# Kernel optimization log

Hardware: AMD Instinct MI355X
Metric: run time of the kernel (lower is better)

## Reference

```python
import jax, jax.numpy as jnp
import numpy as np

N_ATOMS = 262144
N_MOL = 8192       # number of molecules (segments)
MAX_Z = 100        # atomic number vocabulary
MODEL_DIMS = 1024
OUTPUT_DIMS = 1


def setup_inputs() -> dict:
    key = jax.random.key(0)
    k1, k2, k3, k4, k5, k6, k7 = jax.random.split(key, 7)
    atomic_numbers = jax.random.randint(k1, (N_ATOMS,), 0, MAX_Z, dtype=jnp.int64 if jax.config.jax_enable_x64 else jnp.int32)
    pos = jax.random.normal(k2, (N_ATOMS, 3), dtype=jnp.float32)
    batch = jnp.sort(jax.random.randint(k3, (N_ATOMS,), 0, N_MOL, dtype=atomic_numbers.dtype))
    # learned parameters of atom_rr (embedding + position projection) and the head Linear
    embed = jax.random.normal(k4, (MAX_Z, MODEL_DIMS), dtype=jnp.float32) * 0.02
    w_pos = jax.random.normal(k5, (3, MODEL_DIMS), dtype=jnp.float32) * 0.02
    w = jax.random.normal(k6, (MODEL_DIMS, OUTPUT_DIMS), dtype=jnp.float32) * 0.02
    b = jnp.zeros((OUTPUT_DIMS,), dtype=jnp.float32)
    return {"atomic_numbers": atomic_numbers, "pos": pos, "batch": batch,
            "embed": embed, "w_pos": w_pos, "w": w, "b": b}


def reference(atomic_numbers, pos, batch, embed, w_pos, w, b):
    # Vectorized replacement for the per-molecule Python loop:
    # per-atom features, then segment-sum over molecule ids (data.batch).
    feats = embed[atomic_numbers] + pos @ w_pos          # [N_atoms, D]
    reduced = jax.ops.segment_sum(feats, batch, num_segments=N_MOL)  # [N_mol, D]
    return reduced @ w + b                               # [N_mol, output_dims]
```

## Files before the change

kernel.cpp:

```cpp
#include <hip/hip_runtime.h>

#define N_ATOMS 262144
#define N_MOL 8192
#define MAX_Z 100
#define MODEL_DIMS 1024


__global__ void prep_kernel(const float* __restrict__ embed,
                            const float* __restrict__ w_pos,
                            const float* __restrict__ w,
                            const float* __restrict__ b,
                            float* __restrict__ ewpw,
                            float* __restrict__ out) {
    const int blk = blockIdx.x;
    const int tid = threadIdx.x;
    __shared__ float red[256];

    if (blk < MAX_Z + 3) {
        const float* row = (blk < MAX_Z) ? (embed + (size_t)blk * MODEL_DIMS)
                                         : (w_pos + (size_t)(blk - MAX_Z) * MODEL_DIMS);
        float s = 0.f;
        for (int j = tid; j < MODEL_DIMS; j += 256)
            s += row[j] * w[j];
        red[tid] = s;
        __syncthreads();
        for (int off = 128; off > 0; off >>= 1) {
            if (tid < off) red[tid] += red[tid + off];
            __syncthreads();
        }
        if (tid == 0) ewpw[blk] = red[0];
    } else {
        const float bv = b[0];
        for (int i = tid; i < N_MOL; i += 256)
            out[i] = bv;
    }
}

__global__ void atom_kernel(const int* __restrict__ z,
                            const float* __restrict__ pos,
                            const int* __restrict__ batch,
                            const float* __restrict__ ewpw,
                            float* __restrict__ out) {
    const int i = blockIdx.x * blockDim.x + threadIdx.x;
    const float pw0 = ewpw[MAX_Z + 0];
    const float pw1 = ewpw[MAX_Z + 1];
    const float pw2 = ewpw[MAX_Z + 2];

    const int   id = batch[i];
    const int   zi = z[i];
    const float p0 = pos[3 * (size_t)i + 0];
    const float p1 = pos[3 * (size_t)i + 1];
    const float p2 = pos[3 * (size_t)i + 2];

    float v = ewpw[zi] + p0 * pw0 + p1 * pw1 + p2 * pw2;

    const int lane = threadIdx.x & 63;
    #pragma unroll
    for (int off = 1; off < 64; off <<= 1) {
        float vu = __shfl_up(v, off);
        int   iu = __shfl_up(id, off);
        if (lane >= off && iu == id) v += vu;
    }
    const int idn = __shfl_down(id, 1);
    const bool seg_last = (lane == 63) || (idn != id);
    if (seg_last) atomicAdd(&out[id], v);
}

extern "C" void kernel_launch(void* const* d_in, const int* in_sizes, int n_in,
                              void* d_out, int out_size, void* d_ws, size_t ws_size,
                              hipStream_t stream) {
    const int*   atomic_numbers = (const int*)d_in[0];
    const float* pos            = (const float*)d_in[1];
    const int*   batch          = (const int*)d_in[2];
    const float* embed          = (const float*)d_in[3];
    const float* w_pos          = (const float*)d_in[4];
    const float* w              = (const float*)d_in[5];
    const float* b              = (const float*)d_in[6];
    float*       out            = (float*)d_out;
    float*       ewpw           = (float*)d_ws;

    prep_kernel<<<MAX_Z + 4, 256, 0, stream>>>(embed, w_pos, w, b, ewpw, out);

    atom_kernel<<<N_ATOMS / 256, 256, 0, stream>>>(atomic_numbers, pos, batch,
                                                   ewpw, out);
}
```

Before: 11.62 us.

## Fuse prep and atom kernels into one persistent kernel with grid barrier

Merges the weight-dot-product prep kernel and the per-atom segment-reduction kernel into one 256-block launch. A global atomic counter acts as a grid-wide barrier between the two phases. Each block then handles 1024 atoms, four wave-sized chunks per wave, and reads the projected table from LDS. The aim is to drop one kernel launch and the gap between launches. In exchange it adds a spin-wait barrier that requires all 256 blocks to be co-resident, plus counter-reset logic.

Measured after the change: 27.06 us. +132.8%, slower.

```diff
diff --git a/kernel.cpp b/kernel.cpp
--- a/kernel.cpp
+++ b/kernel.cpp
@@ -3,67 +3,100 @@
 #define N_ATOMS 262144
 #define N_MOL 8192
 #define MAX_Z 100
-#define MODEL_DIMS 1024
+#define D 1024
+#define NBLK 256
+#define NTHR 256
+#define NDOT (MAX_Z + 3)
 
+__device__ int g_ready = 0;
+__device__ int g_done  = 0;
 
-__global__ void prep_kernel(const float* __restrict__ embed,
-                            const float* __restrict__ w_pos,
-                            const float* __restrict__ w,
-                            const float* __restrict__ b,
-                            float* __restrict__ ewpw,
-                            float* __restrict__ out) {
-    const int blk = blockIdx.x;
-    const int tid = threadIdx.x;
-    __shared__ float red[256];
+__global__ __launch_bounds__(NTHR) void fused_energy_kernel(
+    const int* __restrict__ z, const float* __restrict__ pos,
+    const int* __restrict__ batch,
+    const float* __restrict__ embed, const float* __restrict__ w_pos,
+    const float* __restrict__ w, const float* __restrict__ b,
+    float* __restrict__ out, float* __restrict__ ewpw)
+{
+    const int blk = blockIdx.x, tid = threadIdx.x;
+    __shared__ float red[NTHR];
+    __shared__ float ew_lds[NDOT];
 
-    if (blk < MAX_Z + 3) {
-        const float* row = (blk < MAX_Z) ? (embed + (size_t)blk * MODEL_DIMS)
-                                         : (w_pos + (size_t)(blk - MAX_Z) * MODEL_DIMS);
+    if (blk < NDOT) {
+        const float* row = (blk < MAX_Z) ? embed + (size_t)blk * D
+                                         : w_pos + (size_t)(blk - MAX_Z) * D;
         float s = 0.f;
-        for (int j = tid; j < MODEL_DIMS; j += 256)
-            s += row[j] * w[j];
+        for (int j = tid; j < D; j += NTHR) s += row[j] * w[j];
         red[tid] = s;
         __syncthreads();
-        for (int off = 128; off > 0; off >>= 1) {
+        for (int off = NTHR / 2; off > 0; off >>= 1) {
             if (tid < off) red[tid] += red[tid + off];
             __syncthreads();
         }
-        if (tid == 0) ewpw[blk] = red[0];
-    } else {
+        if (tid == 0)
+            __hip_atomic_store(&ewpw[blk], red[0], __ATOMIC_RELAXED,
+                               __HIP_MEMORY_SCOPE_AGENT);
+    }
+    {
         const float bv = b[0];
-        for (int i = tid; i < N_MOL; i += 256)
-            out[i] = bv;
+        const int base = blk * (N_MOL / NBLK);
+        if (tid < N_MOL / NBLK) out[base + tid] = bv;
     }
-}
 
-__global__ void atom_kernel(const int* __restrict__ z,
-                            const float* __restrict__ pos,
-                            const int* __restrict__ batch,
-                            const float* __restrict__ ewpw,
-                            float* __restrict__ out) {
-    const int i = blockIdx.x * blockDim.x + threadIdx.x;
-    const float pw0 = ewpw[MAX_Z + 0];
-    const float pw1 = ewpw[MAX_Z + 1];
-    const float pw2 = ewpw[MAX_Z + 2];
+    __syncthreads();
+    if (tid == 0) {
+        __threadfence();
+        __hip_atomic_fetch_add(&g_ready, 1, __ATOMIC_RELEASE,
+                               __HIP_MEMORY_SCOPE_AGENT);
+        while (__hip_atomic_load(&g_ready, __ATOMIC_RELAXED,
+                                 __HIP_MEMORY_SCOPE_AGENT) < NBLK)
+            __builtin_amdgcn_s_sleep(2);
+    }
+    __syncthreads();
 
-    const int   id = batch[i];
-    const int   zi = z[i];
-    const float p0 = pos[3 * (size_t)i + 0];
-    const float p1 = pos[3 * (size_t)i + 1];
-    const float p2 = pos[3 * (size_t)i + 2];
+    if (tid < NDOT)
+        ew_lds[tid] = __hip_atomic_load(&ewpw[tid], __ATOMIC_RELAXED,
+                                        __HIP_MEMORY_SCOPE_AGENT);
+    __syncthreads();
 
-    float v = ewpw[zi] + p0 * pw0 + p1 * pw1 + p2 * pw2;
+    const float pw0 = ew_lds[MAX_Z + 0];
+    const float pw1 = ew_lds[MAX_Z + 1];
+    const float pw2 = ew_lds[MAX_Z + 2];
+    const int lane = tid & 63;
+    const int wv   = tid >> 6;
+    const int wbase = blk * (N_ATOMS / NBLK) + wv * 256;
 
-    const int lane = threadIdx.x & 63;
     #pragma unroll
-    for (int off = 1; off < 64; off <<= 1) {
-        float vu = __shfl_up(v, off);
-        int   iu = __shfl_up(id, off);
-        if (lane >= off && iu == id) v += vu;
+    for (int t = 0; t < 4; ++t) {
+        const int i  = wbase + t * 64 + lane;
+        const int id = batch[i];
+        const int zi = z[i];
+        const float p0 = pos[3 * (size_t)i + 0];
+        const float p1 = pos[3 * (size_t)i + 1];
+        const float p2 = pos[3 * (size_t)i + 2];
+        float v = ew_lds[zi] + p0 * pw0 + p1 * pw1 + p2 * pw2;
+
+        #pragma unroll
+        for (int off = 1; off < 64; off <<= 1) {
+            float vu = __shfl_up(v, off);
+            int   iu = __shfl_up(id, off);
+            if (lane >= off && iu == id) v += vu;
+        }
+        const int idn = __shfl_down(id, 1);
+        if (lane == 63 || idn != id) atomicAdd(&out[id], v);
     }
-    const int idn = __shfl_down(id, 1);
-    const bool seg_last = (lane == 63) || (idn != id);
-    if (seg_last) atomicAdd(&out[id], v);
+
+    __syncthreads();
+    if (tid == 0) {
+        int old = __hip_atomic_fetch_add(&g_done, 1, __ATOMIC_ACQ_REL,
+                                         __HIP_MEMORY_SCOPE_AGENT);
+        if (old == NBLK - 1) {
+            __hip_atomic_store(&g_ready, 0, __ATOMIC_RELAXED,
+                               __HIP_MEMORY_SCOPE_AGENT);
+            __hip_atomic_store(&g_done, 0, __ATOMIC_RELAXED,
+                               __HIP_MEMORY_SCOPE_AGENT);
+        }
+    }
 }
 
 extern "C" void kernel_launch(void* const* d_in, const int* in_sizes, int n_in,
@@ -79,8 +112,6 @@
     float*       out            = (float*)d_out;
     float*       ewpw           = (float*)d_ws;
 
-    prep_kernel<<<MAX_Z + 4, 256, 0, stream>>>(embed, w_pos, w, b, ewpw, out);
-
-    atom_kernel<<<N_ATOMS / 256, 256, 0, stream>>>(atomic_numbers, pos, batch,
-                                                   ewpw, out);
+    fused_energy_kernel<<<NBLK, NTHR, 0, stream>>>(
+        atomic_numbers, pos, batch, embed, w_pos, w, b, out, ewpw);
 }
```

## Fuse table prep and segment sum into one kernel with per-block molecule ranges

Applied to the files above, without the earlier changes.

Merges the two launches into a single kernel. Each of 128 blocks recomputes the 103-entry dot-product table (embed·w, w_pos·w) redundantly in shared memory, then binary-searches the sorted batch array with wave ballots to find the atom range for its 64 molecules. It accumulates into shared memory and writes out once with the bias, removing global atomics and the out initialisation pass. The cost is redundant table computation per block (about 400KB of reads each, mostly from L2), and only 128 blocks to stream 262K atoms, which may underfill the GPU.

Result: slower. 14.59 us (+25.5%).

```diff
diff --git a/kernel.cpp b/kernel.cpp
--- a/kernel.cpp
+++ b/kernel.cpp
@@ -1,69 +1,104 @@
 #include <hip/hip_runtime.h>
 
 #define N_ATOMS 262144
-#define N_MOL 8192
-#define MAX_Z 100
-#define MODEL_DIMS 1024
+#define N_MOL   8192
+#define MAX_Z   100
+#define D       1024
+#define NDOT    (MAX_Z + 3)
+#define NBLK    128
+#define NTHR    512
+#define MPB     (N_MOL / NBLK)
+#define WAVES   (NTHR / 64)
 
+__global__ __launch_bounds__(NTHR) void fused_energy_kernel(
+    const int* __restrict__ z, const float* __restrict__ pos,
+    const int* __restrict__ batch,
+    const float* __restrict__ embed, const float* __restrict__ w_pos,
+    const float* __restrict__ w, const float* __restrict__ b,
+    float* __restrict__ out)
+{
+    const int blk  = blockIdx.x, tid = threadIdx.x;
+    const int lane = tid & 63,   wv  = tid >> 6;
+    __shared__ float tab[NDOT];
+    __shared__ float mol[MPB];
+    __shared__ int   bounds[2];
 
-__global__ void prep_kernel(const float* __restrict__ embed,
-                            const float* __restrict__ w_pos,
-                            const float* __restrict__ w,
-                            const float* __restrict__ b,
-                            float* __restrict__ ewpw,
-                            float* __restrict__ out) {
-    const int blk = blockIdx.x;
-    const int tid = threadIdx.x;
-    __shared__ float red[256];
+    if (tid < MPB) mol[tid] = 0.f;
 
-    if (blk < MAX_Z + 3) {
-        const float* row = (blk < MAX_Z) ? (embed + (size_t)blk * MODEL_DIMS)
-                                         : (w_pos + (size_t)(blk - MAX_Z) * MODEL_DIMS);
+    const int mol_base = blk * MPB;
+
+    if (wv < 2) {
+        const int V = mol_base + wv * MPB;
+        int lower;
+        int v1 = batch[lane * 4096];
+        int c1 = __popcll(__ballot(v1 < V));
+        if (c1 == 0) {
+            lower = 0;
+        } else {
+            int base1 = (c1 - 1) * 4096;
+            int idx2  = base1 + (lane + 1) * 64;
+            int v2    = (idx2 < N_ATOMS) ? batch[idx2] : 0x7fffffff;
+            int c2    = __popcll(__ballot(v2 < V));
+            int base2 = base1 + c2 * 64;
+            int idx3  = base2 + 1 + lane;
+            int v3    = (idx3 < N_ATOMS) ? batch[idx3] : 0x7fffffff;
+            int c3    = __popcll(__ballot(v3 < V));
+            lower = base2 + 1 + c3;
+        }
+        if (lane == 0) bounds[wv] = lower;
+    }
+
+    float4 wc[4];
+    #pragma unroll
+    for (int k = 0; k < 4; ++k)
+        wc[k] = *(const float4*)&w[4 * lane + 256 * k];
+
+    for (int r = wv; r < NDOT; r += WAVES) {
+        const float* row = (r < MAX_Z) ? embed + (size_t)r * D
+                                       : w_pos + (size_t)(r - MAX_Z) * D;
         float s = 0.f;
-        for (int j = tid; j < MODEL_DIMS; j += 256)
-            s += row[j] * w[j];
-        red[tid] = s;
-        __syncthreads();
-        for (int off = 128; off > 0; off >>= 1) {
-            if (tid < off) red[tid] += red[tid + off];
-            __syncthreads();
+        #pragma unroll
+        for (int k = 0; k < 4; ++k) {
+            float4 rv = *(const float4*)&row[4 * lane + 256 * k];
+            s += rv.x * wc[k].x + rv.y * wc[k].y + rv.z * wc[k].z + rv.w * wc[k].w;
         }
-        if (tid == 0) ewpw[blk] = red[0];
-    } else {
-        const float bv = b[0];
-        for (int i = tid; i < N_MOL; i += 256)
-            out[i] = bv;
+        #pragma unroll
+        for (int off = 32; off > 0; off >>= 1)
+            s += __shfl_xor(s, off);
+        if (lane == 0) tab[r] = s;
     }
-}
+    __syncthreads();
 
-__global__ void atom_kernel(const int* __restrict__ z,
-                            const float* __restrict__ pos,
-                            const int* __restrict__ batch,
-                            const float* __restrict__ ewpw,
-                            float* __restrict__ out) {
-    const int i = blockIdx.x * blockDim.x + threadIdx.x;
-    const float pw0 = ewpw[MAX_Z + 0];
-    const float pw1 = ewpw[MAX_Z + 1];
-    const float pw2 = ewpw[MAX_Z + 2];
+    const int lower = bounds[0], upper = bounds[1];
+    const float pw0 = tab[MAX_Z + 0];
+    const float pw1 = tab[MAX_Z + 1];
+    const float pw2 = tab[MAX_Z + 2];
 
-    const int   id = batch[i];
-    const int   zi = z[i];
-    const float p0 = pos[3 * (size_t)i + 0];
-    const float p1 = pos[3 * (size_t)i + 1];
-    const float p2 = pos[3 * (size_t)i + 2];
+    for (int base = lower; base < upper; base += NTHR) {
+        const int  i     = base + tid;
+        const bool valid = i < upper;
+        const int  ii    = valid ? i : (upper - 1);
 
-    float v = ewpw[zi] + p0 * pw0 + p1 * pw1 + p2 * pw2;
+        const int   id = valid ? batch[ii] : 0x7fffffff;
+        const int   zi = z[ii];
+        const float p0 = pos[3 * (size_t)ii + 0];
+        const float p1 = pos[3 * (size_t)ii + 1];
+        const float p2 = pos[3 * (size_t)ii + 2];
+        float v = valid ? (tab[zi] + p0 * pw0 + p1 * pw1 + p2 * pw2) : 0.f;
 
-    const int lane = threadIdx.x & 63;
-    #pragma unroll
-    for (int off = 1; off < 64; off <<= 1) {
-        float vu = __shfl_up(v, off);
-        int   iu = __shfl_up(id, off);
-        if (lane >= off && iu == id) v += vu;
+        #pragma unroll
+        for (int off = 1; off < 64; off <<= 1) {
+            float vu = __shfl_up(v, off);
+            int   iu = __shfl_up(id, off);
+            if (lane >= off && iu == id) v += vu;
+        }
+        const int idn = __shfl_down(id, 1);
+        if (valid && (lane == 63 || idn != id))
+            atomicAdd(&mol[id - mol_base], v);
     }
-    const int idn = __shfl_down(id, 1);
-    const bool seg_last = (lane == 63) || (idn != id);
-    if (seg_last) atomicAdd(&out[id], v);
+    __syncthreads();
+
+    if (tid < MPB) out[mol_base + tid] = b[0] + mol[tid];
 }
 
 extern "C" void kernel_launch(void* const* d_in, const int* in_sizes, int n_in,
@@ -77,10 +112,7 @@
     const float* w              = (const float*)d_in[5];
     const float* b              = (const float*)d_in[6];
     float*       out            = (float*)d_out;
-    float*       ewpw           = (float*)d_ws;
 
-    prep_kernel<<<MAX_Z + 4, 256, 0, stream>>>(embed, w_pos, w, b, ewpw, out);
-
-    atom_kernel<<<N_ATOMS / 256, 256, 0, stream>>>(atomic_numbers, pos, batch,
-                                                   ewpw, out);
+    fused_energy_kernel<<<NBLK, NTHR, 0, stream>>>(
+        atomic_numbers, pos, batch, embed, w_pos, w, b, out);
 }
```
